# Kernel optimization log

Hardware: AMD Instinct MI355X
Metric: run time of the kernel (lower is better)

Reference implementation:

```python
import jax, jax.numpy as jnp
import numpy as np

NUM_NODES = 100000
NUM_EDGES = 1600000
NUM_GRAPHS = 512
IN_F = 128
BN_EPS = 1e-5


def setup_inputs() -> dict:
    key = jax.random.key(0)
    ks = jax.random.split(key, 8)
    x = jax.random.normal(ks[0], (NUM_NODES, IN_F), dtype=jnp.float32)
    edge_index = jax.random.randint(ks[1], (2, NUM_EDGES), 0, NUM_NODES, dtype=jnp.int64)
    batch = jnp.sort(jax.random.randint(ks[2], (NUM_NODES,), 0, NUM_GRAPHS, dtype=jnp.int64))

    def glorot(k, shape):
        lim = np.sqrt(6.0 / (shape[0] + shape[1]))
        return jax.random.uniform(k, shape, jnp.float32, -lim, lim)

    return {
        "x": x,
        "edge_index": edge_index,
        "batch": batch,
        "W1": glorot(ks[3], (IN_F, 128)),
        "b1": jnp.zeros((128,), jnp.float32),
        "W2": glorot(ks[4], (128, 64)),
        "b2": jnp.zeros((64,), jnp.float32),
        "gamma": jnp.ones((64,), jnp.float32),
        "beta": jnp.zeros((64,), jnp.float32),
        "Wo1": glorot(ks[5], (64, 24)),
        "bo1": jnp.zeros((24,), jnp.float32),
        "Wo2": glorot(ks[6], (24, 1)),
        "bo2": jnp.zeros((1,), jnp.float32),
    }


def gcn_conv(x, src, dst, W, b, n):
    # PyG GCNConv: add self-loops, symmetric D^{-1/2} A D^{-1/2} normalization,
    # linear transform, scatter-add aggregation at destination, then bias.
    deg = jax.ops.segment_sum(jnp.ones_like(dst, jnp.float32), dst, num_segments=n)
    dis = jnp.where(deg > 0, jax.lax.rsqrt(deg), 0.0)
    norm = dis[src] * dis[dst]  # [E+N]
    xw = x @ W                  # [N, out]
    msg = xw[src] * norm[:, None]
    return jax.ops.segment_sum(msg, dst, num_segments=n) + b


def reference(x, edge_index, batch, W1, b1, W2, b2, gamma, beta, Wo1, bo1, Wo2, bo2):
    n = NUM_NODES
    loop = jnp.arange(n, dtype=edge_index.dtype)
    src = jnp.concatenate([edge_index[0], loop])  # self-loops appended
    dst = jnp.concatenate([edge_index[1], loop])

    h1 = jax.nn.relu(gcn_conv(x, src, dst, W1, b1, n))
    h2 = jax.nn.relu(gcn_conv(h1, src, dst, W2, b2, n))

    pooled = jax.ops.segment_sum(h2, batch, num_segments=NUM_GRAPHS)  # [G, 64]
    h = jax.lax.stop_gradient(pooled)

    # BatchNorm1d in training mode: batch statistics over the graph dim.
    mean = jnp.mean(pooled, axis=0)
    var = jnp.var(pooled, axis=0)
    xn = (pooled - mean) * jax.lax.rsqrt(var + BN_EPS) * gamma + beta

    out = jax.nn.relu(xn @ Wo1 + bo1) @ Wo2 + bo2  # [G, 1]
    return out, h
```

## Files before the change

kernel.cpp:

```cpp
#include <hip/hip_runtime.h>
#include <math.h>

#define N_NODES 100000
#define N_EDGES 1600000
#define N_GRAPHS 512
#define BN_EPS 1e-5f

#define NBUCKET 1024
#define NBUCKET_USED ((N_NODES + 127) / 128)
#define SLOT 2560
#define BCHUNK 8192
#define NCHUNKS ((N_EDGES + BCHUNK - 1) / BCHUNK)

typedef unsigned int uint;
typedef unsigned short ushort;
typedef unsigned char uchar;
typedef _Float16 f16;
typedef _Float16 f16x8 __attribute__((ext_vector_type(8)));
typedef float f32x4 __attribute__((ext_vector_type(4)));
typedef float f32x2 __attribute__((ext_vector_type(2)));

constexpr size_t OFF_BCUR = 0;
constexpr size_t OFF_DIS  = 4096;
constexpr size_t OFF_ROW  = 404096;
constexpr size_t OFF_END  = 804096;
constexpr size_t OFF_WT   = 1204096;
constexpr size_t OFF_BIN  = 1253248;
constexpr size_t OFF_CSR  = 11739008;
constexpr size_t OFF_P    = 22224768;
constexpr size_t OFF_Q    = 28624768;
constexpr size_t OFF_H2   = 41424768;

__device__ __forceinline__ uint packf16(float a, float b) {
    union { f16 h[2]; uint u; } z;
    z.h[0] = (f16)a; z.h[1] = (f16)b;
    return z.u;
}
__device__ __forceinline__ uchar f2fp8(float v) {
    return (uchar)(__builtin_amdgcn_cvt_pk_fp8_f32(v, v, 0, false) & 0xff);
}

__global__ __launch_bounds__(256) void init_prep(const float* __restrict__ W1,
                                                 const float* __restrict__ W2,
                                                 f16* __restrict__ wT,
                                                 int* __restrict__ bcur) {
    int b = blockIdx.x;
    if (b == 96) {
        int t = threadIdx.x;
        bcur[t] = 0; bcur[t + 256] = 0; bcur[t + 512] = 0; bcur[t + 768] = 0;
        return;
    }
    int tid = b * 256 + threadIdx.x;
    if (tid < 16384) {
        int n = tid >> 7, k = tid & 127;
        wT[tid] = (f16)W1[k * 128 + n];
    } else {
        int t = tid - 16384;
        int n = t >> 7, k = t & 127;
        wT[tid] = (f16)W2[k * 64 + n];
    }
}

__global__ __launch_bounds__(1024) void bin_scatter(const int* __restrict__ src,
                                                    const int* __restrict__ dst,
                                                    int* __restrict__ bcur,
                                                    uint* __restrict__ binned) {
    constexpr int REG = BCHUNK / 1024;
    __shared__ int hist[NBUCKET];
    __shared__ int base[NBUCKET];
    int t = threadIdx.x;
    int e0 = blockIdx.x * BCHUNK;
    int lim = N_EDGES - e0;

    hist[t] = 0;
    __syncthreads();

    int ds[REG], ss[REG];
#pragma unroll
    for (int i = 0; i < REG; ++i) {
        int idx = t + i * 1024;
        if (idx < lim) {
            ds[i] = dst[e0 + idx];
            ss[i] = src[e0 + idx];
            atomicAdd(&hist[ds[i] >> 7], 1);
        }
    }
    __syncthreads();

    int h = hist[t];
    base[t] = h ? atomicAdd(&bcur[t], h) : 0;
    hist[t] = 0;
    __syncthreads();

#pragma unroll
    for (int i = 0; i < REG; ++i) {
        int idx = t + i * 1024;
        if (idx < lim) {
            int b = ds[i] >> 7;
            int pos = b * SLOT + base[b] + atomicAdd(&hist[b], 1);
            binned[pos] = ((uint)ss[i] << 7) | (uint)(ds[i] & 127);
        }
    }
}

__global__ __launch_bounds__(256) void csr_from_bins(const uint* __restrict__ binned,
                                                     const int* __restrict__ bcur,
                                                     int* __restrict__ row_start,
                                                     int* __restrict__ row_end,
                                                     float* __restrict__ dis,
                                                     int* __restrict__ csr_src) {
    __shared__ int cnt[128];
    __shared__ int ex[128];
    int t = threadIdx.x;
    int b = blockIdx.x;
    if (t < 128) cnt[t] = 0;
    __syncthreads();
    int base = b * SLOT;
    int nb = bcur[b];
    for (int i = t; i < nb; i += 256)
        atomicAdd(&cnt[binned[base + i] & 127u], 1);
    __syncthreads();
    if (t < 128) ex[t] = cnt[t];
    __syncthreads();
    for (int off = 1; off < 128; off <<= 1) {
        int v = (t < 128 && t >= off) ? ex[t - off] : 0;
        __syncthreads();
        if (t < 128) ex[t] += v;
        __syncthreads();
    }
    if (t < 128) {
        int c = cnt[t];
        ex[t] -= c;
        int node = b * 128 + t;
        if (node < N_NODES) {
            int rs = base + ex[t];
            row_start[node] = rs;
            row_end[node] = rs + c;
            dis[node] = rsqrtf((float)(c + 1));
        }
        cnt[t] = 0;
    }
    __syncthreads();
    for (int i = t; i < nb; i += 256) {
        uint p = binned[base + i];
        int s = (int)(p >> 7);
        int d = (int)(p & 127u);
        int pos = base + ex[d] + atomicAdd(&cnt[d], 1);
        csr_src[pos] = s;
    }
}

__global__ __launch_bounds__(256) void gemm_mfma1(const float* __restrict__ X,
                                                  const float* __restrict__ dis,
                                                  const f16* __restrict__ Bt,
                                                  uchar* __restrict__ Y) {
    constexpr int NT = 8;
    constexpr int PITCH = 136;
    __shared__ f16 sA[64 * PITCH];
    __shared__ f16 sB[128 * PITCH];
    int tid = threadIdx.x;
    int n0 = blockIdx.x * 64;

    for (int i = tid; i < 64 * 16; i += 256) {
        int r = i >> 4, c = i & 15;
        int n = n0 + r;
        uint4 pk = make_uint4(0, 0, 0, 0);
        if (n < N_NODES) {
            const float4* px = (const float4*)(X + (size_t)n * 128);
            float4 u = px[c * 2], v = px[c * 2 + 1];
            float d = dis[n];
            pk.x = packf16(u.x * d, u.y * d);
            pk.y = packf16(u.z * d, u.w * d);
            pk.z = packf16(v.x * d, v.y * d);
            pk.w = packf16(v.z * d, v.w * d);
        }
        *(uint4*)&sA[r * PITCH + c * 8] = pk;
    }
    for (int i = tid; i < 128 * 16; i += 256) {
        int r = i >> 4, c = i & 15;
        *(uint4*)&sB[r * PITCH + c * 8] = ((const uint4*)(Bt + r * 128))[c];
    }
    __syncthreads();

    int lane = tid & 63, wave = tid >> 6;
    int l15 = lane & 15, q = lane >> 4;
    int m0 = wave * 16;
    f32x4 acc[NT];
#pragma unroll
    for (int nt = 0; nt < NT; ++nt) acc[nt] = (f32x4){0.f, 0.f, 0.f, 0.f};

    const f16* pa = &sA[(m0 + l15) * PITCH + q * 8];
    const f16* pb = &sB[l15 * PITCH + q * 8];
#pragma unroll
    for (int kk = 0; kk < 4; ++kk) {
        f16x8 a = *(const f16x8*)(pa + kk * 32);
#pragma unroll
        for (int nt = 0; nt < NT; ++nt) {
            f16x8 b = *(const f16x8*)(pb + nt * 16 * PITCH + kk * 32);
            acc[nt] = __builtin_amdgcn_mfma_f32_16x16x32_f16(a, b, acc[nt], 0, 0, 0);
        }
    }

    int row_base = n0 + m0 + q * 4;
#pragma unroll
    for (int nt = 0; nt < NT; ++nt) {
#pragma unroll
        for (int r = 0; r < 4; ++r) {
            int row = row_base + r;
            if (row < N_NODES)
                Y[(size_t)row * 128 + nt * 16 + l15] = f2fp8(acc[nt][r]);
        }
    }
}

__global__ __launch_bounds__(256) void aggregate1_fused(const ushort* __restrict__ M,
                                                        const int* __restrict__ row_start,
                                                        const int* __restrict__ row_end,
                                                        const int* __restrict__ csr_src,
                                                        const float* __restrict__ dis,
                                                        const float* __restrict__ bias,
                                                        const f16* __restrict__ W2t,
                                                        uchar* __restrict__ M2) {
    constexpr int PITCH = 136;
    constexpr int HP = 130;
    __shared__ f16 sB[64 * PITCH];
    __shared__ f16 sH[16 * HP];
    int tid = threadIdx.x;
    for (int i = tid; i < 64 * 16; i += 256) {
        int r = i >> 4, c = i & 15;
        *(uint4*)&sB[r * PITCH + c * 8] = ((const uint4*)(W2t + r * 128))[c];
    }
    int wv = __builtin_amdgcn_readfirstlane((int)(tid >> 6));
    int lane = tid & 63;
    int n0 = blockIdx.x * 16;

    for (int i = 0; i < 4; ++i) {
        int r = wv * 4 + i;
        int n = n0 + r;
        float dn = dis[n];
        int e0 = row_start[n], e1 = row_end[n];
        f32x2 t0 = __builtin_amdgcn_cvt_pk_f32_fp8((int)M[(size_t)n * 64 + lane], false);
        float a0 = t0.x, a1 = t0.y, b0 = 0.f, b1v = 0.f;
        int e = e0;
        for (; e + 16 <= e1; e += 16) {
            int s[16];
#pragma unroll
            for (int j = 0; j < 16; ++j) s[j] = csr_src[e + j];
            ushort v[16];
#pragma unroll
            for (int j = 0; j < 16; ++j) v[j] = M[(size_t)s[j] * 64 + lane];
#pragma unroll
            for (int j = 0; j < 16; ++j) {
                f32x2 f = __builtin_amdgcn_cvt_pk_f32_fp8((int)v[j], false);
                if (j & 1) { b0 += f.x; b1v += f.y; } else { a0 += f.x; a1 += f.y; }
            }
        }
        for (; e + 8 <= e1; e += 8) {
            int s[8];
#pragma unroll
            for (int j = 0; j < 8; ++j) s[j] = csr_src[e + j];
            ushort v[8];
#pragma unroll
            for (int j = 0; j < 8; ++j) v[j] = M[(size_t)s[j] * 64 + lane];
#pragma unroll
            for (int j = 0; j < 8; ++j) {
                f32x2 f = __builtin_amdgcn_cvt_pk_f32_fp8((int)v[j], false);
                if (j & 1) { b0 += f.x; b1v += f.y; } else { a0 += f.x; a1 += f.y; }
            }
        }
        for (; e + 4 <= e1; e += 4) {
            int s0 = csr_src[e], s1 = csr_src[e + 1], s2 = csr_src[e + 2], s3 = csr_src[e + 3];
            ushort v0 = M[(size_t)s0 * 64 + lane];
            ushort v1 = M[(size_t)s1 * 64 + lane];
            ushort v2 = M[(size_t)s2 * 64 + lane];
            ushort v3 = M[(size_t)s3 * 64 + lane];
            f32x2 f0 = __builtin_amdgcn_cvt_pk_f32_fp8((int)v0, false);
            f32x2 f1 = __builtin_amdgcn_cvt_pk_f32_fp8((int)v1, false);
            f32x2 f2 = __builtin_amdgcn_cvt_pk_f32_fp8((int)v2, false);
            f32x2 f3 = __builtin_amdgcn_cvt_pk_f32_fp8((int)v3, false);
            a0 += f0.x + f1.x; a1 += f0.y + f1.y;
            b0 += f2.x + f3.x; b1v += f2.y + f3.y;
        }
        for (; e < e1; ++e) {
            f32x2 f = __builtin_amdgcn_cvt_pk_f32_fp8((int)M[(size_t)csr_src[e] * 64 + lane], false);
            a0 += f.x; a1 += f.y;
        }
        a0 += b0; a1 += b1v;
        a0 = fmaxf(fmaf(a0, dn, bias[2 * lane]), 0.f) * dn;
        a1 = fmaxf(fmaf(a1, dn, bias[2 * lane + 1]), 0.f) * dn;
        *(uint*)&sH[r * HP + 2 * lane] = packf16(a0, a1);
    }
    __syncthreads();

    int l15 = lane & 15, q = lane >> 4;
    f32x4 acc = (f32x4){0.f, 0.f, 0.f, 0.f};
    const f16* pa = &sH[l15 * HP + q * 8];
    const f16* pb = &sB[(wv * 16 + l15) * PITCH + q * 8];
#pragma unroll
    for (int kk = 0; kk < 4; ++kk) {
        f16x8 a = *(const f16x8*)(pa + kk * 32);
        f16x8 b = *(const f16x8*)(pb + kk * 32);
        acc = __builtin_amdgcn_mfma_f32_16x16x32_f16(a, b, acc, 0, 0, 0);
    }
    int row_base = n0 + q * 4;
#pragma unroll
    for (int rr = 0; rr < 4; ++rr)
        M2[(size_t)(row_base + rr) * 64 + wv * 16 + l15] = f2fp8(acc[rr]);
}

__global__ __launch_bounds__(256) void aggregate2(const uchar* __restrict__ M,
                                                  const int* __restrict__ row_start,
                                                  const int* __restrict__ row_end,
                                                  const int* __restrict__ csr_src,
                                                  const float* __restrict__ dis,
                                                  const float* __restrict__ bias,
                                                  ushort* __restrict__ out) {
    int wv = __builtin_amdgcn_readfirstlane((int)(threadIdx.x >> 6));
    int n = blockIdx.x * 4 + wv;
    if (n >= N_NODES) return;
    int lane = threadIdx.x & 63;
    float dn = dis[n];
    int e0 = row_start[n], e1 = row_end[n];
    float a0 = __builtin_amdgcn_cvt_f32_fp8((int)M[(size_t)n * 64 + lane], 0);
    float a1 = 0.f;
    int e = e0;
    for (; e + 16 <= e1; e += 16) {
        int s[16];
#pragma unroll
        for (int j = 0; j < 16; ++j) s[j] = csr_src[e + j];
        uchar v[16];
#pragma unroll
        for (int j = 0; j < 16; ++j) v[j] = M[(size_t)s[j] * 64 + lane];
#pragma unroll
        for (int j = 0; j < 16; ++j) {
            float f = __builtin_amdgcn_cvt_f32_fp8((int)v[j], 0);
            if (j & 1) a1 += f; else a0 += f;
        }
    }
    for (; e + 8 <= e1; e += 8) {
        int s[8];
#pragma unroll
        for (int j = 0; j < 8; ++j) s[j] = csr_src[e + j];
        uchar v[8];
#pragma unroll
        for (int j = 0; j < 8; ++j) v[j] = M[(size_t)s[j] * 64 + lane];
#pragma unroll
        for (int j = 0; j < 8; ++j) {
            float f = __builtin_amdgcn_cvt_f32_fp8((int)v[j], 0);
            if (j & 1) a1 += f; else a0 += f;
        }
    }
    for (; e + 4 <= e1; e += 4) {
        int s0 = csr_src[e], s1 = csr_src[e + 1], s2 = csr_src[e + 2], s3 = csr_src[e + 3];
        float v0 = __builtin_amdgcn_cvt_f32_fp8((int)M[(size_t)s0 * 64 + lane], 0);
        float v1 = __builtin_amdgcn_cvt_f32_fp8((int)M[(size_t)s1 * 64 + lane], 0);
        float v2 = __builtin_amdgcn_cvt_f32_fp8((int)M[(size_t)s2 * 64 + lane], 0);
        float v3 = __builtin_amdgcn_cvt_f32_fp8((int)M[(size_t)s3 * 64 + lane], 0);
        a0 += v0 + v1; a1 += v2 + v3;
    }
    for (; e < e1; ++e)
        a0 += __builtin_amdgcn_cvt_f32_fp8((int)M[(size_t)csr_src[e] * 64 + lane], 0);
    a0 += a1;
    a0 = fmaxf(fmaf(a0, dn, bias[lane]), 0.f);
    union { f16 h; ushort u; } z;
    z.h = (f16)a0;
    out[(size_t)n * 64 + lane] = z.u;
}

__global__ __launch_bounds__(256) void pool_graphs(const ushort* __restrict__ H,
                                                   const int* __restrict__ batch,
                                                   float* __restrict__ pooled) {
    __shared__ float part[4][64];
    int g = blockIdx.x;
    int tid = threadIdx.x;
    int wv = tid >> 6, lane = tid & 63;
    int lo = 0, hi = N_NODES;
    while (lo < hi) { int mid = (lo + hi) >> 1; if (batch[mid] < g) lo = mid + 1; else hi = mid; }
    int start = lo;
    hi = N_NODES;
    while (lo < hi) { int mid = (lo + hi) >> 1; if (batch[mid] < g + 1) lo = mid + 1; else hi = mid; }
    int end = lo;
    const f16* rows = (const f16*)H;
    float a0 = 0.f, a1 = 0.f;
    int i = start + wv;
    for (; i + 12 < end; i += 16) {
        a0 += (float)rows[(size_t)i * 64 + lane] + (float)rows[(size_t)(i + 4) * 64 + lane];
        a1 += (float)rows[(size_t)(i + 8) * 64 + lane] + (float)rows[(size_t)(i + 12) * 64 + lane];
    }
    for (; i < end; i += 4) a0 += (float)rows[(size_t)i * 64 + lane];
    part[wv][lane] = a0 + a1;
    __syncthreads();
    if (wv == 0)
        pooled[g * 64 + lane] = part[0][lane] + part[1][lane] + part[2][lane] + part[3][lane];
}

__global__ __launch_bounds__(512) void bn_head(const float* __restrict__ pooled,
                                               const float* __restrict__ gamma,
                                               const float* __restrict__ beta,
                                               const float* __restrict__ Wo1,
                                               const float* __restrict__ bo1,
                                               const float* __restrict__ Wo2,
                                               const float* __restrict__ bo2,
                                               float* __restrict__ out) {
    __shared__ float sW1[64 * 24];
    __shared__ float sW2[24];
    __shared__ float sb1[24];
    __shared__ float ssc[64];
    __shared__ float ssh[64];
    int tid = threadIdx.x;
    for (int i = tid; i < 64 * 24; i += 512) sW1[i] = Wo1[i];
    if (tid >= 64 && tid < 88) { int k = tid - 64; sW2[k] = Wo2[k]; sb1[k] = bo1[k]; }
    if (tid < 64) {
        float s = 0.f, s2 = 0.f;
        for (int g = 0; g < N_GRAPHS; ++g) {
            float v = pooled[g * 64 + tid];
            s += v;
            s2 = fmaf(v, v, s2);
        }
        float mean = s * (1.0f / N_GRAPHS);
        float var = s2 * (1.0f / N_GRAPHS) - mean * mean;
        float istd = rsqrtf(var + BN_EPS);
        float sc = gamma[tid] * istd;
        ssc[tid] = sc;
        ssh[tid] = beta[tid] - mean * sc;
    }
    __syncthreads();
    int g = tid;
    float xn[64];
    const float* pr = pooled + g * 64;
#pragma unroll
    for (int j = 0; j < 64; ++j) xn[j] = fmaf(pr[j], ssc[j], ssh[j]);
    float o = bo2[0];
#pragma unroll 4
    for (int k = 0; k < 24; ++k) {
        float h = sb1[k];
#pragma unroll
        for (int j = 0; j < 64; ++j) h = fmaf(xn[j], sW1[j * 24 + k], h);
        o = fmaf(fmaxf(h, 0.f), sW2[k], o);
    }
    out[g] = o;
}

extern "C" void kernel_launch(void* const* d_in, const int* in_sizes, int n_in,
                              void* d_out, int out_size, void* d_ws, size_t ws_size,
                              hipStream_t stream) {
    const float* x     = (const float*)d_in[0];
    const int*   ei    = (const int*)d_in[1];
    const int*   batch = (const int*)d_in[2];
    const float* W1    = (const float*)d_in[3];
    const float* b1    = (const float*)d_in[4];
    const float* W2    = (const float*)d_in[5];
    const float* b2    = (const float*)d_in[6];
    const float* gamma = (const float*)d_in[7];
    const float* beta  = (const float*)d_in[8];
    const float* Wo1   = (const float*)d_in[9];
    const float* bo1   = (const float*)d_in[10];
    const float* Wo2   = (const float*)d_in[11];
    const float* bo2   = (const float*)d_in[12];
    float* out = (float*)d_out;
    char* ws = (char*)d_ws;

    const int* srcv = ei;
    const int* dstv = ei + N_EDGES;
    int*    bcur     = (int*)(ws + OFF_BCUR);
    float*  dis      = (float*)(ws + OFF_DIS);
    int*    row_start= (int*)(ws + OFF_ROW);
    int*    row_end  = (int*)(ws + OFF_END);
    f16*    wT       = (f16*)(ws + OFF_WT);
    uint*   binned   = (uint*)(ws + OFF_BIN);
    int*    csr_src  = (int*)(ws + OFF_CSR);
    uchar*  bufP     = (uchar*)(ws + OFF_P);
    uchar*  bufQ     = (uchar*)(ws + OFF_Q);
    ushort* h2       = (ushort*)(ws + OFF_H2);
    float*  pooled   = out + N_GRAPHS;

    init_prep<<<97, 256, 0, stream>>>(W1, W2, wT, bcur);
    bin_scatter<<<NCHUNKS, 1024, 0, stream>>>(srcv, dstv, bcur, binned);
    csr_from_bins<<<NBUCKET_USED, 256, 0, stream>>>(binned, bcur, row_start, row_end, dis, csr_src);

    int gblocks = (N_NODES + 63) / 64;
    gemm_mfma1<<<gblocks, 256, 0, stream>>>(x, dis, wT, bufQ);
    aggregate1_fused<<<N_NODES / 16, 256, 0, stream>>>((const ushort*)bufQ, row_start, row_end,
                                                       csr_src, dis, b1, wT + 16384, bufP);
    aggregate2<<<(N_NODES + 3) / 4, 256, 0, stream>>>(bufP, row_start, row_end, csr_src, dis, b2,
                                                      h2);

    pool_graphs<<<N_GRAPHS, 256, 0, stream>>>(h2, batch, pooled);
    bn_head<<<1, 512, 0, stream>>>(pooled, gamma, beta, Wo1, bo1, Wo2, bo2, out);
}
```

Measured before the change: 276.5 us.

## Fuse second-layer aggregation into per-graph pooling kernel

Replaces the separate layer-2 aggregation kernel and pooling kernel with one kernel that runs one block per graph. Each wave aggregates its nodes' neighbours, applies bias and ReLU, and accumulates straight into a per-graph sum. This removes the intermediate h2 buffer write and reread and one kernel launch. In exchange, parallelism drops to 512 blocks, and each wave walks its graph's nodes one after another, which could reduce latency hiding for the random gathers.

```diff
diff --git a/kernel.cpp b/kernel.cpp
--- a/kernel.cpp
+++ b/kernel.cpp
@@ -29,7 +29,6 @@
 constexpr size_t OFF_CSR  = 11739008;
 constexpr size_t OFF_P    = 22224768;
 constexpr size_t OFF_Q    = 28624768;
-constexpr size_t OFF_H2   = 41424768;
 
 __device__ __forceinline__ uint packf16(float a, float b) {
     union { f16 h[2]; uint u; } z;
@@ -308,69 +307,15 @@
         M2[(size_t)(row_base + rr) * 64 + wv * 16 + l15] = f2fp8(acc[rr]);
 }
 
-__global__ __launch_bounds__(256) void aggregate2(const uchar* __restrict__ M,
-                                                  const int* __restrict__ row_start,
-                                                  const int* __restrict__ row_end,
-                                                  const int* __restrict__ csr_src,
-                                                  const float* __restrict__ dis,
-                                                  const float* __restrict__ bias,
-                                                  ushort* __restrict__ out) {
-    int wv = __builtin_amdgcn_readfirstlane((int)(threadIdx.x >> 6));
-    int n = blockIdx.x * 4 + wv;
-    if (n >= N_NODES) return;
-    int lane = threadIdx.x & 63;
-    float dn = dis[n];
-    int e0 = row_start[n], e1 = row_end[n];
-    float a0 = __builtin_amdgcn_cvt_f32_fp8((int)M[(size_t)n * 64 + lane], 0);
-    float a1 = 0.f;
-    int e = e0;
-    for (; e + 16 <= e1; e += 16) {
-        int s[16];
-#pragma unroll
-        for (int j = 0; j < 16; ++j) s[j] = csr_src[e + j];
-        uchar v[16];
-#pragma unroll
-        for (int j = 0; j < 16; ++j) v[j] = M[(size_t)s[j] * 64 + lane];
-#pragma unroll
-        for (int j = 0; j < 16; ++j) {
-            float f = __builtin_amdgcn_cvt_f32_fp8((int)v[j], 0);
-            if (j & 1) a1 += f; else a0 += f;
-        }
-    }
-    for (; e + 8 <= e1; e += 8) {
-        int s[8];
-#pragma unroll
-        for (int j = 0; j < 8; ++j) s[j] = csr_src[e + j];
-        uchar v[8];
-#pragma unroll
-        for (int j = 0; j < 8; ++j) v[j] = M[(size_t)s[j] * 64 + lane];
-#pragma unroll
-        for (int j = 0; j < 8; ++j) {
-            float f = __builtin_amdgcn_cvt_f32_fp8((int)v[j], 0);
-            if (j & 1) a1 += f; else a0 += f;
-        }
-    }
-    for (; e + 4 <= e1; e += 4) {
-        int s0 = csr_src[e], s1 = csr_src[e + 1], s2 = csr_src[e + 2], s3 = csr_src[e + 3];
-        float v0 = __builtin_amdgcn_cvt_f32_fp8((int)M[(size_t)s0 * 64 + lane], 0);
-        float v1 = __builtin_amdgcn_cvt_f32_fp8((int)M[(size_t)s1 * 64 + lane], 0);
-        float v2 = __builtin_amdgcn_cvt_f32_fp8((int)M[(size_t)s2 * 64 + lane], 0);
-        float v3 = __builtin_amdgcn_cvt_f32_fp8((int)M[(size_t)s3 * 64 + lane], 0);
-        a0 += v0 + v1; a1 += v2 + v3;
-    }
-    for (; e < e1; ++e)
-        a0 += __builtin_amdgcn_cvt_f32_fp8((int)M[(size_t)csr_src[e] * 64 + lane], 0);
-    a0 += a1;
-    a0 = fmaxf(fmaf(a0, dn, bias[lane]), 0.f);
-    union { f16 h; ushort u; } z;
-    z.h = (f16)a0;
-    out[(size_t)n * 64 + lane] = z.u;
-}
-
-__global__ __launch_bounds__(256) void pool_graphs(const ushort* __restrict__ H,
-                                                   const int* __restrict__ batch,
-                                                   float* __restrict__ pooled) {
-    __shared__ float part[4][64];
+__global__ __launch_bounds__(512) void agg2_pool(const uchar* __restrict__ M,
+                                                 const int* __restrict__ row_start,
+                                                 const int* __restrict__ row_end,
+                                                 const int* __restrict__ csr_src,
+                                                 const float* __restrict__ dis,
+                                                 const float* __restrict__ bias,
+                                                 const int* __restrict__ batch,
+                                                 float* __restrict__ pooled) {
+    __shared__ float part[8][64];
     int g = blockIdx.x;
     int tid = threadIdx.x;
     int wv = tid >> 6, lane = tid & 63;
@@ -380,18 +325,61 @@
     hi = N_NODES;
     while (lo < hi) { int mid = (lo + hi) >> 1; if (batch[mid] < g + 1) lo = mid + 1; else hi = mid; }
     int end = lo;
-    const f16* rows = (const f16*)H;
-    float a0 = 0.f, a1 = 0.f;
-    int i = start + wv;
-    for (; i + 12 < end; i += 16) {
-        a0 += (float)rows[(size_t)i * 64 + lane] + (float)rows[(size_t)(i + 4) * 64 + lane];
-        a1 += (float)rows[(size_t)(i + 8) * 64 + lane] + (float)rows[(size_t)(i + 12) * 64 + lane];
-    }
-    for (; i < end; i += 4) a0 += (float)rows[(size_t)i * 64 + lane];
-    part[wv][lane] = a0 + a1;
-    __syncthreads();
-    if (wv == 0)
-        pooled[g * 64 + lane] = part[0][lane] + part[1][lane] + part[2][lane] + part[3][lane];
+    float bl = bias[lane];
+    float pacc = 0.f;
+    for (int nn = start + wv; nn < end; nn += 8) {
+        int n = __builtin_amdgcn_readfirstlane(nn);
+        float dn = dis[n];
+        int e0 = row_start[n], e1 = row_end[n];
+        float a0 = __builtin_amdgcn_cvt_f32_fp8((int)M[(size_t)n * 64 + lane], 0);
+        float a1 = 0.f;
+        int e = e0;
+        for (; e + 16 <= e1; e += 16) {
+            int s[16];
+#pragma unroll
+            for (int j = 0; j < 16; ++j) s[j] = csr_src[e + j];
+            uchar v[16];
+#pragma unroll
+            for (int j = 0; j < 16; ++j) v[j] = M[(size_t)s[j] * 64 + lane];
+#pragma unroll
+            for (int j = 0; j < 16; ++j) {
+                float f = __builtin_amdgcn_cvt_f32_fp8((int)v[j], 0);
+                if (j & 1) a1 += f; else a0 += f;
+            }
+        }
+        for (; e + 8 <= e1; e += 8) {
+            int s[8];
+#pragma unroll
+            for (int j = 0; j < 8; ++j) s[j] = csr_src[e + j];
+            uchar v[8];
+#pragma unroll
+            for (int j = 0; j < 8; ++j) v[j] = M[(size_t)s[j] * 64 + lane];
+#pragma unroll
+            for (int j = 0; j < 8; ++j) {
+                float f = __builtin_amdgcn_cvt_f32_fp8((int)v[j], 0);
+                if (j & 1) a1 += f; else a0 += f;
+            }
+        }
+        for (; e + 4 <= e1; e += 4) {
+            int s0 = csr_src[e], s1 = csr_src[e + 1], s2 = csr_src[e + 2], s3 = csr_src[e + 3];
+            float v0 = __builtin_amdgcn_cvt_f32_fp8((int)M[(size_t)s0 * 64 + lane], 0);
+            float v1 = __builtin_amdgcn_cvt_f32_fp8((int)M[(size_t)s1 * 64 + lane], 0);
+            float v2 = __builtin_amdgcn_cvt_f32_fp8((int)M[(size_t)s2 * 64 + lane], 0);
+            float v3 = __builtin_amdgcn_cvt_f32_fp8((int)M[(size_t)s3 * 64 + lane], 0);
+            a0 += v0 + v1; a1 += v2 + v3;
+        }
+        for (; e < e1; ++e)
+            a0 += __builtin_amdgcn_cvt_f32_fp8((int)M[(size_t)csr_src[e] * 64 + lane], 0);
+        a0 += a1;
+        pacc += fmaxf(fmaf(a0, dn, bl), 0.f);
+    }
+    part[wv][lane] = pacc;
+    __syncthreads();
+    if (wv == 0) {
+        float s = part[0][lane] + part[1][lane] + part[2][lane] + part[3][lane]
+                + part[4][lane] + part[5][lane] + part[6][lane] + part[7][lane];
+        pooled[g * 64 + lane] = s;
+    }
 }
 
 __global__ __launch_bounds__(512) void bn_head(const float* __restrict__ pooled,
@@ -471,7 +459,6 @@
     int*    csr_src  = (int*)(ws + OFF_CSR);
     uchar*  bufP     = (uchar*)(ws + OFF_P);
     uchar*  bufQ     = (uchar*)(ws + OFF_Q);
-    ushort* h2       = (ushort*)(ws + OFF_H2);
     float*  pooled   = out + N_GRAPHS;
 
     init_prep<<<97, 256, 0, stream>>>(W1, W2, wT, bcur);
@@ -482,9 +469,7 @@
     gemm_mfma1<<<gblocks, 256, 0, stream>>>(x, dis, wT, bufQ);
     aggregate1_fused<<<N_NODES / 16, 256, 0, stream>>>((const ushort*)bufQ, row_start, row_end,
                                                        csr_src, dis, b1, wT + 16384, bufP);
-    aggregate2<<<(N_NODES + 3) / 4, 256, 0, stream>>>(bufP, row_start, row_end, csr_src, dis, b2,
-                                                      h2);
-
-    pool_graphs<<<N_GRAPHS, 256, 0, stream>>>(h2, batch, pooled);
+    agg2_pool<<<N_GRAPHS, 512, 0, stream>>>(bufP, row_start, row_end, csr_src, dis, b2, batch,
+                                            pooled);
     bn_head<<<1, 512, 0, stream>>>(pooled, gamma, beta, Wo1, bo1, Wo2, bo2, out);
 }
```

New measurement: 288.0 us. 4.1% more time.

## Fuse graph pooling into second aggregation via atomic adds

Applied to the files above, without the earlier changes.

Removes the separate pooling kernel and the fp16 h2 intermediate buffer. Each node's final activation is accumulated directly into the per-graph pooled vector with float atomicAdd, and init_prep gets extra blocks that zero the pooled buffer. This saves a full write and re-read of the node features plus one launch. In exchange it adds many contended atomics and makes the summation order nondeterministic.

```diff
diff --git a/kernel.cpp b/kernel.cpp
--- a/kernel.cpp
+++ b/kernel.cpp
@@ -29,7 +29,6 @@
 constexpr size_t OFF_CSR  = 11739008;
 constexpr size_t OFF_P    = 22224768;
 constexpr size_t OFF_Q    = 28624768;
-constexpr size_t OFF_H2   = 41424768;
 
 __device__ __forceinline__ uint packf16(float a, float b) {
     union { f16 h[2]; uint u; } z;
@@ -43,11 +42,18 @@
 __global__ __launch_bounds__(256) void init_prep(const float* __restrict__ W1,
                                                  const float* __restrict__ W2,
                                                  f16* __restrict__ wT,
-                                                 int* __restrict__ bcur) {
+                                                 int* __restrict__ bcur,
+                                                 float* __restrict__ pooled) {
     int b = blockIdx.x;
     if (b == 96) {
         int t = threadIdx.x;
         bcur[t] = 0; bcur[t + 256] = 0; bcur[t + 512] = 0; bcur[t + 768] = 0;
+        return;
+    }
+    if (b >= 97) {
+        int base = (b - 97) * 4096 + threadIdx.x * 16;
+#pragma unroll
+        for (int i = 0; i < 16; ++i) pooled[base + i] = 0.f;
         return;
     }
     int tid = b * 256 + threadIdx.x;
@@ -314,7 +320,8 @@
                                                   const int* __restrict__ csr_src,
                                                   const float* __restrict__ dis,
                                                   const float* __restrict__ bias,
-                                                  ushort* __restrict__ out) {
+                                                  const int* __restrict__ batch,
+                                                  float* __restrict__ pooled) {
     int wv = __builtin_amdgcn_readfirstlane((int)(threadIdx.x >> 6));
     int n = blockIdx.x * 4 + wv;
     if (n >= N_NODES) return;
@@ -362,36 +369,8 @@
         a0 += __builtin_amdgcn_cvt_f32_fp8((int)M[(size_t)csr_src[e] * 64 + lane], 0);
     a0 += a1;
     a0 = fmaxf(fmaf(a0, dn, bias[lane]), 0.f);
-    union { f16 h; ushort u; } z;
-    z.h = (f16)a0;
-    out[(size_t)n * 64 + lane] = z.u;
-}
-
-__global__ __launch_bounds__(256) void pool_graphs(const ushort* __restrict__ H,
-                                                   const int* __restrict__ batch,
-                                                   float* __restrict__ pooled) {
-    __shared__ float part[4][64];
-    int g = blockIdx.x;
-    int tid = threadIdx.x;
-    int wv = tid >> 6, lane = tid & 63;
-    int lo = 0, hi = N_NODES;
-    while (lo < hi) { int mid = (lo + hi) >> 1; if (batch[mid] < g) lo = mid + 1; else hi = mid; }
-    int start = lo;
-    hi = N_NODES;
-    while (lo < hi) { int mid = (lo + hi) >> 1; if (batch[mid] < g + 1) lo = mid + 1; else hi = mid; }
-    int end = lo;
-    const f16* rows = (const f16*)H;
-    float a0 = 0.f, a1 = 0.f;
-    int i = start + wv;
-    for (; i + 12 < end; i += 16) {
-        a0 += (float)rows[(size_t)i * 64 + lane] + (float)rows[(size_t)(i + 4) * 64 + lane];
-        a1 += (float)rows[(size_t)(i + 8) * 64 + lane] + (float)rows[(size_t)(i + 12) * 64 + lane];
-    }
-    for (; i < end; i += 4) a0 += (float)rows[(size_t)i * 64 + lane];
-    part[wv][lane] = a0 + a1;
-    __syncthreads();
-    if (wv == 0)
-        pooled[g * 64 + lane] = part[0][lane] + part[1][lane] + part[2][lane] + part[3][lane];
+    int g = batch[n];
+    atomicAdd(&pooled[g * 64 + lane], a0);
 }
 
 __global__ __launch_bounds__(512) void bn_head(const float* __restrict__ pooled,
@@ -471,10 +450,9 @@
     int*    csr_src  = (int*)(ws + OFF_CSR);
     uchar*  bufP     = (uchar*)(ws + OFF_P);
     uchar*  bufQ     = (uchar*)(ws + OFF_Q);
-    ushort* h2       = (ushort*)(ws + OFF_H2);
     float*  pooled   = out + N_GRAPHS;
 
-    init_prep<<<97, 256, 0, stream>>>(W1, W2, wT, bcur);
+    init_prep<<<105, 256, 0, stream>>>(W1, W2, wT, bcur, pooled);
     bin_scatter<<<NCHUNKS, 1024, 0, stream>>>(srcv, dstv, bcur, binned);
     csr_from_bins<<<NBUCKET_USED, 256, 0, stream>>>(binned, bcur, row_start, row_end, dis, csr_src);
 
@@ -483,8 +461,6 @@
     aggregate1_fused<<<N_NODES / 16, 256, 0, stream>>>((const ushort*)bufQ, row_start, row_end,
                                                        csr_src, dis, b1, wT + 16384, bufP);
     aggregate2<<<(N_NODES + 3) / 4, 256, 0, stream>>>(bufP, row_start, row_end, csr_src, dis, b2,
-                                                      h2);
-
-    pool_graphs<<<N_GRAPHS, 256, 0, stream>>>(h2, batch, pooled);
+                                                      batch, pooled);
     bn_head<<<1, 512, 0, stream>>>(pooled, gamma, beta, Wo1, bo1, Wo2, bo2, out);
 }
```

After: 281.5 us. Within noise of the previous version (+1.8%).
